# Kernel optimization log

Measured on AMD Instinct MI355X. Metric: run time of the kernel, lower is better.

The kernel has to match this reference:

```python
import jax, jax.numpy as jnp
import numpy as np

D_MODEL = 1024
NUM_HEADS = 16
ROPE_BASE = 10000.0


def _rope_sincos(T, head_dim, dtype):
    # angles[t, i] = t / base**(2i/head_dim), i in [0, head_dim//2)
    pos = jnp.arange(T, dtype=jnp.float32)[:, None]              # [T, 1]
    inv_freq = 1.0 / (ROPE_BASE ** (jnp.arange(0, head_dim, 2, dtype=jnp.float32) / head_dim))
    angles = pos * inv_freq                                       # [T, half]
    sin = jnp.sin(angles).astype(dtype)[None, :, None, :]         # [1, T, 1, half]
    cos = jnp.cos(angles).astype(dtype)[None, :, None, :]
    return sin, cos


def _apply_rope(x, sin, cos):
    # x: [B, T, H, head_dim]; deinterleave even/odd lanes, rotate, concat halves
    x1, x2 = x[..., ::2], x[..., 1::2]                            # [B, T, H, half] each
    return jnp.concatenate([x1 * cos - x2 * sin, x1 * sin + x2 * cos], axis=-1)


def setup_inputs() -> dict:
    key = jax.random.key(0)
    ks = jax.random.split(key, 5)
    B, T, D = 2, 2048, D_MODEL
    s = 0.02
    return {
        "x": jax.random.normal(ks[0], (B, T, D), dtype=jnp.float32),
        "w_qkv": jax.random.normal(ks[1], (3 * D, D), dtype=jnp.float32) * s,
        "b_qkv": jnp.zeros((3 * D,), dtype=jnp.float32),
        "w_out": jax.random.normal(ks[2], (D, D), dtype=jnp.float32) * s,
        "b_out": jnp.zeros((D,), dtype=jnp.float32),
    }


def reference(x, w_qkv, b_qkv, w_out, b_out):
    B, T, D = x.shape
    H = NUM_HEADS
    hd = D // H
    scale = hd ** -0.5

    qkv = (x @ w_qkv.T + b_qkv).reshape(B, T, 3, H, hd)
    q, k, v = qkv[:, :, 0], qkv[:, :, 1], qkv[:, :, 2]            # [B, T, H, hd]

    sin, cos = _rope_sincos(T, hd, x.dtype)
    q = _apply_rope(q, sin, cos)
    k = _apply_rope(k, sin, cos)

    scores = jnp.einsum("bthd,bshd->bhts", q, k) * scale          # [B, H, T, T]
    weights = jax.nn.softmax(scores, axis=-1)
    out = jnp.einsum("bhts,bshd->bthd", weights, v)               # [B, T, H, hd]
    out = out.reshape(B, T, D)
    return out @ w_out.T + b_out
```

## Files before the change

kernel.cpp:

```cpp
#include <hip/hip_runtime.h>
#include <cstdint>
#include <cstddef>

typedef __attribute__((ext_vector_type(8))) short short8;
typedef __attribute__((ext_vector_type(8))) __bf16 bf16x8;
typedef __attribute__((ext_vector_type(4))) float f32x4;
typedef __attribute__((ext_vector_type(16))) float f32x16;
typedef __attribute__((ext_vector_type(4))) unsigned int uint32x4;

#define LOG2E 1.44269504088896340736f

__device__ __forceinline__ unsigned short f2bf(float f) {
    unsigned int u = __builtin_bit_cast(unsigned int, f);
    u += 0x7fffu + ((u >> 16) & 1u);
    return (unsigned short)(u >> 16);
}

__device__ __forceinline__ f32x4 zero4() {
    f32x4 z; z.x = 0.f; z.y = 0.f; z.z = 0.f; z.w = 0.f; return z;
}
__device__ __forceinline__ f32x16 zero16() {
    f32x16 z;
    #pragma unroll
    for (int i = 0; i < 16; ++i) z[i] = 0.f;
    return z;
}

__device__ __forceinline__ f32x4 mfma16(short8 a, short8 b, f32x4 c) {
    return __builtin_amdgcn_mfma_f32_16x16x32_bf16(
        __builtin_bit_cast(bf16x8, a), __builtin_bit_cast(bf16x8, b), c, 0, 0, 0);
}
__device__ __forceinline__ f32x16 mfma32(short8 a, short8 b, f32x16 c) {
    return __builtin_amdgcn_mfma_f32_32x32x16_bf16(
        __builtin_bit_cast(bf16x8, a), __builtin_bit_cast(bf16x8, b), c, 0, 0, 0);
}

__device__ __forceinline__ unsigned int cvt_pk_bf16(float lo, float hi) {
    unsigned int r;
    asm("v_cvt_pk_bf16_f32 %0, %1, %2" : "=v"(r) : "v"(lo), "v"(hi));
    return r;
}

__device__ __forceinline__ uint2 permswap(unsigned x, unsigned y) {
#if __has_builtin(__builtin_amdgcn_permlane32_swap)
    auto r = __builtin_amdgcn_permlane32_swap(x, y, false, false);
    return make_uint2(r[0], r[1]);
#else
    int lane = threadIdx.x & 63;
    unsigned sy = __shfl_xor(y, 32), sx = __shfl_xor(x, 32);
    return make_uint2((lane < 32) ? x : sy, (lane < 32) ? sx : y);
#endif
}
__device__ __forceinline__ float red_max32(float v) {
    unsigned u = __builtin_bit_cast(unsigned, v);
    uint2 p = permswap(u, u);
    return fmaxf(__builtin_bit_cast(float, p.x), __builtin_bit_cast(float, p.y));
}

__device__ __forceinline__ void gload_lds16(const void* g, void* l, int lane) {
#if __has_builtin(__builtin_amdgcn_global_load_lds)
    __builtin_amdgcn_global_load_lds(
        (const __attribute__((address_space(1))) void*)g,
        (__attribute__((address_space(3))) void*)l, 16, 0, 0);
    (void)lane;
#else
    reinterpret_cast<int4*>(l)[lane] = *reinterpret_cast<const int4*>(g);
#endif
}

__global__ __launch_bounds__(256) void prep_kernel(
    const float* __restrict__ x, const float* __restrict__ wq,
    const float* __restrict__ wo,
    unsigned short* __restrict__ xb, unsigned short* __restrict__ wqb,
    unsigned short* __restrict__ wob, float2* __restrict__ tab) {
    const int S0 = 1048576, S1 = 786432, S2 = 262144;
    int i = blockIdx.x * 256 + threadIdx.x;
    const float* src; unsigned short* dst; int j;
    if (i < S0) { src = x; dst = xb; j = i; }
    else if (i < S0 + S1) { src = wq; dst = wqb; j = i - S0; }
    else if (i < S0 + S1 + S2) { src = wo; dst = wob; j = i - S0 - S1; }
    else {
        int idx = i - (S0 + S1 + S2);
        if (idx < 2048 * 32) {
            int t = idx >> 5, ii = idx & 31;
            float inv_freq = powf(10000.0f, -(float)ii / 32.0f);
            float ang = (float)t * inv_freq;
            tab[idx] = make_float2(cosf(ang), sinf(ang));
        }
        return;
    }
    float4 v = reinterpret_cast<const float4*>(src)[j];
    ushort4 o;
    o.x = f2bf(v.x); o.y = f2bf(v.y); o.z = f2bf(v.z); o.w = f2bf(v.w);
    reinterpret_cast<ushort4*>(dst)[j] = o;
}

template<int BM, int BN, int WMG, int WNG>
__device__ __forceinline__ void gemm_mainloop(
    const unsigned short* __restrict__ A, const unsigned short* __restrict__ B,
    int K, int m0, int n0, char* As, char* Bs,
    f32x4 (&acc)[BM / (WMG * 16)][BN / (WNG * 16)]) {
    constexpr int MT = BM / (WMG * 16), NTT = BN / (WNG * 16);
    constexpr int CA = BM / 64, CB = BN / 64;
    constexpr int ABUF = BM * 128, BBUF = BN * 128;
    int tid = threadIdx.x;
    int wave = tid >> 6, lane = tid & 63;
    int wm = wave / WNG, wn = wave % WNG;
    int g = lane >> 4, c = lane & 15;
    const int NS = K >> 6;

    auto stage = [&](int buf, int k0) {
        #pragma unroll
        for (int i = 0; i < CA; ++i) {
            int call = wave * CA + i;
            int s = call * 64 + lane;
            int row = s >> 3, c8 = s & 7;
            int csw = (c8 ^ (row & 7)) << 3;
            gload_lds16(A + (size_t)(m0 + row) * K + k0 + csw,
                        As + buf * ABUF + call * 1024, lane);
        }
        #pragma unroll
        for (int i = 0; i < CB; ++i) {
            int call = wave * CB + i;
            int s = call * 64 + lane;
            int row = s >> 3, c8 = s & 7;
            int csw = (c8 ^ (row & 7)) << 3;
            gload_lds16(B + (size_t)(n0 + row) * K + k0 + csw,
                        Bs + buf * BBUF + call * 1024, lane);
        }
    };

    stage(0, 0);

    #pragma unroll 1
    for (int t = 0; t < NS; ++t) {
        int cur = t & 1;
        asm volatile("s_waitcnt vmcnt(0)" ::: "memory");
        __builtin_amdgcn_s_barrier();
        __builtin_amdgcn_sched_barrier(0);
        if (t + 1 < NS) stage(cur ^ 1, (t + 1) * 64);

        const char* Ac = As + cur * ABUF;
        const char* Bc = Bs + cur * BBUF;
        #pragma unroll
        for (int kg = 0; kg < 2; ++kg) {
            short8 af[MT], bfr[NTT];
            #pragma unroll
            for (int mt = 0; mt < MT; ++mt) {
                int row = wm * (BM / WMG) + mt * 16 + c;
                af[mt] = *reinterpret_cast<const short8*>(Ac +
                    ((row * 128 + kg * 64 + g * 16) ^ ((row & 7) << 4)));
            }
            #pragma unroll
            for (int nt = 0; nt < NTT; ++nt) {
                int row = wn * (BN / WNG) + nt * 16 + c;
                bfr[nt] = *reinterpret_cast<const short8*>(Bc +
                    ((row * 128 + kg * 64 + g * 16) ^ ((row & 7) << 4)));
            }
            __builtin_amdgcn_s_setprio(1);
            #pragma unroll
            for (int mt = 0; mt < MT; ++mt)
                #pragma unroll
                for (int nt = 0; nt < NTT; ++nt)
                    acc[mt][nt] = mfma16(af[mt], bfr[nt], acc[mt][nt]);
            __builtin_amdgcn_s_setprio(0);
        }
    }
}

__global__ __launch_bounds__(512, 2) void qkv_gemm_kernel(
    const unsigned short* __restrict__ X, const unsigned short* __restrict__ W,
    const float* __restrict__ bias, const float2* __restrict__ tab,
    unsigned short* __restrict__ q, unsigned short* __restrict__ k,
    unsigned short* __restrict__ vt) {
    __shared__ char smem[80 * 1024];
    const int K = 1024;
    const float SCL = 0.125f * LOG2E;
    int flat = blockIdx.x;
    int swzb = (flat & 7) * 64 + (flat >> 3);
    int m0 = (swzb >> 4) * 128, n0 = (swzb & 15) * 192;
    f32x4 acc[2][6];
    #pragma unroll
    for (int i = 0; i < 2; ++i)
        #pragma unroll
        for (int j = 0; j < 6; ++j) acc[i][j] = zero4();

    gemm_mainloop<128, 192, 4, 2>(X, W, K, m0, n0, smem, smem + 32768, acc);

    int tid = threadIdx.x;
    int wave = tid >> 6, lane = tid & 63;
    int wm = wave >> 1, wn = wave & 1;
    int g = lane >> 4, c = lane & 15;
    int mbase = m0 + wm * 32, nbase = n0 + wn * 96;
    #pragma unroll
    for (int mt = 0; mt < 2; ++mt) {
        #pragma unroll
        for (int nt = 0; nt < 6; ++nt) {
            f32x4 a = acc[mt][nt];
            int n = nbase + nt * 16 + c;
            int s = n >> 10;
            int h = (n >> 6) & 15;
            int d = n & 63;
            float bn = bias[n];
            #pragma unroll
            for (int r = 0; r < 4; ++r) {
                int m = mbase + mt * 16 + g * 4 + r;
                int bb = m >> 11, t = m & 2047;
                float val = a[r] + bn;
                float partner = __shfl_xor(val, 1);
                int bh = bb * 16 + h;
                if (s == 2) {
                    vt[((size_t)bh * 64 + d) * 2048 + t] = f2bf(val);
                } else {
                    int i2 = d >> 1;
                    float2 cs = tab[t * 32 + i2];
                    float outv; int dout;
                    if ((d & 1) == 0) { outv = val * cs.x - partner * cs.y; dout = i2; }
                    else              { outv = partner * cs.y + val * cs.x; dout = 32 + i2; }
                    if (s == 0) outv *= SCL;
                    (s == 0 ? q : k)[((size_t)bh * 2048 + t) * 64 + dout] = f2bf(outv);
                }
            }
        }
    }
}

__global__ __launch_bounds__(256, 2) void attn_kernel(
    const unsigned short* __restrict__ Q, const unsigned short* __restrict__ Kin,
    const unsigned short* __restrict__ VT, unsigned short* __restrict__ O) {
    __shared__ int4 smem4[65536 / 16];
    char* smem = (char*)smem4;
    const int T = 2048, NT = 16;
    int flat = blockIdx.x + 16 * blockIdx.y;
    int swzb = (flat & 7) * 64 + (flat >> 3);
    int bh = swzb >> 4;
    int qt = swzb & 15;
    int tid = threadIdx.x, wave = tid >> 6, lane = tid & 63;
    int lam = lane & 31, hi = lane >> 5;
    int q = qt * 128 + wave * 32 + lam;

    const unsigned short* Qb = Q + ((size_t)bh * T + q) * 64;
    const unsigned short* Kb = Kin + (size_t)bh * T * 64;
    const unsigned short* VTb = VT + (size_t)bh * 64 * T;

    uint32x4 qtmp[4];
    #pragma unroll
    for (int c4 = 0; c4 < 4; ++c4)
        qtmp[c4] = *reinterpret_cast<const uint32x4*>(Qb + c4 * 16 + hi * 8);
    #pragma unroll
    for (int c4 = 0; c4 < 4; ++c4)
        asm volatile("" : "+v"(qtmp[c4]));
    short8 qf[4];
    #pragma unroll
    for (int c4 = 0; c4 < 4; ++c4) qf[c4] = __builtin_bit_cast(short8, qtmp[c4]);

    short8 ones;
    #pragma unroll
    for (int i = 0; i < 8; ++i) ones[i] = (short)0x3F80;

    f32x16 o0 = zero16(), o1 = zero16(), lacc = zero16();
    float m_run = -1e30f;
    int swz = (lam & 7) << 4;

    char* KsB = smem;
    char* VsB = smem + 32768;

    auto stage = [&](int buf, int t) {
        int j0 = t * 128;
        #pragma unroll
        for (int st = 0; st < 2; ++st) {
            #pragma unroll
            for (int i = 0; i < 2; ++i) {
                int call = wave * 2 + i;
                int s = call * 64 + lane;
                int row = s >> 3, c8 = s & 7;
                int csw = (c8 ^ (row & 7)) << 3;
                gload_lds16(Kb + (size_t)(j0 + st * 64 + row) * 64 + csw,
                            KsB + buf * 16384 + st * 8192 + call * 1024, lane);
                gload_lds16(VTb + (size_t)row * T + j0 + st * 64 + csw,
                            VsB + buf * 16384 + st * 8192 + call * 1024, lane);
            }
        }
    };

    auto subtile = [&](const char* Kc, const char* Vc) {
        f32x16 s0 = zero16(), s1 = zero16();
        __builtin_amdgcn_s_setprio(1);
        #pragma unroll
        for (int c4 = 0; c4 < 4; ++c4) {
            int col = c4 * 32 + hi * 16;
            short8 kf0 = *reinterpret_cast<const short8*>(Kc + ((lam * 128 + col) ^ swz));
            s0 = mfma32(kf0, qf[c4], s0);
            short8 kf1 = *reinterpret_cast<const short8*>(Kc + (((lam + 32) * 128 + col) ^ swz));
            s1 = mfma32(kf1, qf[c4], s1);
        }
        __builtin_amdgcn_s_setprio(0);

        float tm = fmaxf(s0[0], s1[0]);
        #pragma unroll
        for (int r = 1; r < 16; ++r) tm = fmaxf(tm, fmaxf(s0[r], s1[r]));
        float tmax = red_max32(tm);
        if (__any(tmax - m_run > 8.0f)) {
            float mnew = fmaxf(m_run, tmax);
            float alpha = exp2f(m_run - mnew);
            m_run = mnew;
            #pragma unroll
            for (int r = 0; r < 16; ++r) {
                o0[r] *= alpha; o1[r] *= alpha; lacc[r] *= alpha;
            }
        }
        float p0[16], p1[16];
        #pragma unroll
        for (int r = 0; r < 16; ++r) p0[r] = exp2f(s0[r] - m_run);
        #pragma unroll
        for (int r = 0; r < 16; ++r) p1[r] = exp2f(s1[r] - m_run);

        short8 pa[4];
        #pragma unroll
        for (int blk = 0; blk < 2; ++blk) {
            const float* p = blk ? p1 : p0;
            #pragma unroll
            for (int jt = 0; jt < 2; ++jt) {
                unsigned a0 = cvt_pk_bf16(p[jt * 8 + 0], p[jt * 8 + 1]);
                unsigned a1 = cvt_pk_bf16(p[jt * 8 + 2], p[jt * 8 + 3]);
                unsigned b0 = cvt_pk_bf16(p[jt * 8 + 4], p[jt * 8 + 5]);
                unsigned b1 = cvt_pk_bf16(p[jt * 8 + 6], p[jt * 8 + 7]);
                uint2 pr0 = permswap(a0, b0);
                uint2 pr1 = permswap(a1, b1);
                uint4 w;
                w.x = pr0.x;
                w.y = pr1.x;
                w.z = pr0.y;
                w.w = pr1.y;
                pa[blk * 2 + jt] = __builtin_bit_cast(short8, w);
            }
        }

        __builtin_amdgcn_s_setprio(1);
        #pragma unroll
        for (int jt = 0; jt < 4; ++jt) {
            int col = jt * 32 + hi * 16;
            short8 vf0 = *reinterpret_cast<const short8*>(Vc + ((lam * 128 + col) ^ swz));
            o0 = mfma32(vf0, pa[jt], o0);
            short8 vf1 = *reinterpret_cast<const short8*>(Vc + (((lam + 32) * 128 + col) ^ swz));
            o1 = mfma32(vf1, pa[jt], o1);
            lacc = mfma32(ones, pa[jt], lacc);
        }
        __builtin_amdgcn_s_setprio(0);
    };

    stage(0, 0);

    #pragma unroll 1
    for (int t = 0; t < NT; ++t) {
        int cur = t & 1;
        asm volatile("s_waitcnt vmcnt(0)" ::: "memory");
        __builtin_amdgcn_s_barrier();
        __builtin_amdgcn_sched_barrier(0);
        if (t + 1 < NT) stage(cur ^ 1, t + 1);

        subtile(KsB + cur * 16384, VsB + cur * 16384);
        subtile(KsB + cur * 16384 + 8192, VsB + cur * 16384 + 8192);
    }

    float l_run = lacc[0];

    float rinv = 1.0f / l_run;
    int b_ = bh >> 4, h_ = bh & 15;
    unsigned short* Orow = O + ((size_t)(b_ * 2048) + q) * 1024 + h_ * 64;
    #pragma unroll
    for (int rq = 0; rq < 4; ++rq) {
        ushort4 w0, w1;
        w0.x = f2bf(o0[rq * 4 + 0] * rinv);
        w0.y = f2bf(o0[rq * 4 + 1] * rinv);
        w0.z = f2bf(o0[rq * 4 + 2] * rinv);
        w0.w = f2bf(o0[rq * 4 + 3] * rinv);
        w1.x = f2bf(o1[rq * 4 + 0] * rinv);
        w1.y = f2bf(o1[rq * 4 + 1] * rinv);
        w1.z = f2bf(o1[rq * 4 + 2] * rinv);
        w1.w = f2bf(o1[rq * 4 + 3] * rinv);
        int d0 = rq * 8 + hi * 4;
        *reinterpret_cast<ushort4*>(Orow + d0) = w0;
        *reinterpret_cast<ushort4*>(Orow + 32 + d0) = w1;
    }
}

__global__ __launch_bounds__(512, 2) void out_gemm_kernel(
    const unsigned short* __restrict__ Aattn, const unsigned short* __restrict__ W,
    const float* __restrict__ bias, float* __restrict__ out) {
    __shared__ char smem[48 * 1024];
    const int K = 1024, N = 1024;
    int flat = blockIdx.x;
    int swzb = (flat & 7) * 64 + (flat >> 3);
    int m0 = (swzb & 63) * 64, n0 = (swzb >> 6) * 128;
    f32x4 acc[2][2];
    #pragma unroll
    for (int i = 0; i < 2; ++i)
        #pragma unroll
        for (int j = 0; j < 2; ++j) acc[i][j] = zero4();

    gemm_mainloop<64, 128, 2, 4>(Aattn, W, K, m0, n0, smem, smem + 16384, acc);

    int tid = threadIdx.x;
    int wave = tid >> 6, lane = tid & 63;
    int wm = wave >> 2, wn = wave & 3;
    int g = lane >> 4, c = lane & 15;
    int mbase = m0 + wm * 32, nbase = n0 + wn * 32;
    #pragma unroll
    for (int mt = 0; mt < 2; ++mt)
        #pragma unroll
        for (int nt = 0; nt < 2; ++nt) {
            int n = nbase + nt * 16 + c;
            float bn = bias[n];
            #pragma unroll
            for (int r = 0; r < 4; ++r) {
                int m = mbase + mt * 16 + g * 4 + r;
                out[(size_t)m * N + n] = acc[mt][nt][r] + bn;
            }
        }
}

extern "C" void kernel_launch(void* const* d_in, const int* in_sizes, int n_in,
                              void* d_out, int out_size, void* d_ws, size_t ws_size,
                              hipStream_t stream) {
    (void)in_sizes; (void)n_in; (void)out_size; (void)ws_size;
    const float* x     = (const float*)d_in[0];
    const float* w_qkv = (const float*)d_in[1];
    const float* b_qkv = (const float*)d_in[2];
    const float* w_out = (const float*)d_in[3];
    const float* b_out = (const float*)d_in[4];
    float* out = (float*)d_out;

    const int B = 2, T = 2048, D = 1024;
    const int M = B * T;
    const size_t MB = 1024 * 1024;
    (void)D; (void)M;

    char* ws = (char*)d_ws;
    unsigned short* xb    = (unsigned short*)(ws);
    unsigned short* wqkvb = (unsigned short*)(ws + 8 * MB);
    unsigned short* woutb = (unsigned short*)(ws + 14 * MB);
    unsigned short* qb    = (unsigned short*)(ws + 16 * MB);
    unsigned short* kb    = (unsigned short*)(ws + 24 * MB);
    unsigned short* vtb   = (unsigned short*)(ws + 32 * MB);
    unsigned short* attnb = (unsigned short*)(ws + 40 * MB);
    float2* tab           = (float2*)(ws + 48 * MB);

    prep_kernel<<<dim3((2097152 + 65536) / 256), dim3(256), 0, stream>>>(
        x, w_qkv, w_out, xb, wqkvb, woutb, tab);
    qkv_gemm_kernel<<<dim3(512), dim3(512), 0, stream>>>(xb, wqkvb, b_qkv, tab, qb, kb, vtb);
    attn_kernel<<<dim3(T / 128, B * 16), dim3(256), 0, stream>>>(qb, kb, vtb, attnb);
    out_gemm_kernel<<<dim3(512), dim3(512), 0, stream>>>(attnb, woutb, b_out, out);
}
```

Baseline: 140.1 us.

## Merge two 64-key subtiles into one 128-key softmax step with V prefetch

Replaces the two sequential 64-key subtile calls per staged tile with a single 128-key step. All four score MFMA groups are issued together and one row-max reduction and rescale check covers the whole tile. The first half of the V fragments is loaded from LDS before the softmax math so the load latency overlaps with the exp and convert work. This halves the cross-lane max reductions and branch checks per tile, but it raises register pressure (four score accumulators, p arrays, eight V fragments), which may reduce occupancy or cause spills.

```diff
diff --git a/kernel.cpp b/kernel.cpp
--- a/kernel.cpp
+++ b/kernel.cpp
@@ -283,72 +283,6 @@
         }
     };
 
-    auto subtile = [&](const char* Kc, const char* Vc) {
-        f32x16 s0 = zero16(), s1 = zero16();
-        __builtin_amdgcn_s_setprio(1);
-        #pragma unroll
-        for (int c4 = 0; c4 < 4; ++c4) {
-            int col = c4 * 32 + hi * 16;
-            short8 kf0 = *reinterpret_cast<const short8*>(Kc + ((lam * 128 + col) ^ swz));
-            s0 = mfma32(kf0, qf[c4], s0);
-            short8 kf1 = *reinterpret_cast<const short8*>(Kc + (((lam + 32) * 128 + col) ^ swz));
-            s1 = mfma32(kf1, qf[c4], s1);
-        }
-        __builtin_amdgcn_s_setprio(0);
-
-        float tm = fmaxf(s0[0], s1[0]);
-        #pragma unroll
-        for (int r = 1; r < 16; ++r) tm = fmaxf(tm, fmaxf(s0[r], s1[r]));
-        float tmax = red_max32(tm);
-        if (__any(tmax - m_run > 8.0f)) {
-            float mnew = fmaxf(m_run, tmax);
-            float alpha = exp2f(m_run - mnew);
-            m_run = mnew;
-            #pragma unroll
-            for (int r = 0; r < 16; ++r) {
-                o0[r] *= alpha; o1[r] *= alpha; lacc[r] *= alpha;
-            }
-        }
-        float p0[16], p1[16];
-        #pragma unroll
-        for (int r = 0; r < 16; ++r) p0[r] = exp2f(s0[r] - m_run);
-        #pragma unroll
-        for (int r = 0; r < 16; ++r) p1[r] = exp2f(s1[r] - m_run);
-
-        short8 pa[4];
-        #pragma unroll
-        for (int blk = 0; blk < 2; ++blk) {
-            const float* p = blk ? p1 : p0;
-            #pragma unroll
-            for (int jt = 0; jt < 2; ++jt) {
-                unsigned a0 = cvt_pk_bf16(p[jt * 8 + 0], p[jt * 8 + 1]);
-                unsigned a1 = cvt_pk_bf16(p[jt * 8 + 2], p[jt * 8 + 3]);
-                unsigned b0 = cvt_pk_bf16(p[jt * 8 + 4], p[jt * 8 + 5]);
-                unsigned b1 = cvt_pk_bf16(p[jt * 8 + 6], p[jt * 8 + 7]);
-                uint2 pr0 = permswap(a0, b0);
-                uint2 pr1 = permswap(a1, b1);
-                uint4 w;
-                w.x = pr0.x;
-                w.y = pr1.x;
-                w.z = pr0.y;
-                w.w = pr1.y;
-                pa[blk * 2 + jt] = __builtin_bit_cast(short8, w);
-            }
-        }
-
-        __builtin_amdgcn_s_setprio(1);
-        #pragma unroll
-        for (int jt = 0; jt < 4; ++jt) {
-            int col = jt * 32 + hi * 16;
-            short8 vf0 = *reinterpret_cast<const short8*>(Vc + ((lam * 128 + col) ^ swz));
-            o0 = mfma32(vf0, pa[jt], o0);
-            short8 vf1 = *reinterpret_cast<const short8*>(Vc + (((lam + 32) * 128 + col) ^ swz));
-            o1 = mfma32(vf1, pa[jt], o1);
-            lacc = mfma32(ones, pa[jt], lacc);
-        }
-        __builtin_amdgcn_s_setprio(0);
-    };
-
     stage(0, 0);
 
     #pragma unroll 1
@@ -359,8 +293,102 @@
         __builtin_amdgcn_sched_barrier(0);
         if (t + 1 < NT) stage(cur ^ 1, t + 1);
 
-        subtile(KsB + cur * 16384, VsB + cur * 16384);
-        subtile(KsB + cur * 16384 + 8192, VsB + cur * 16384 + 8192);
+        const char* Kc = KsB + cur * 16384;
+        const char* Vc = VsB + cur * 16384;
+
+        f32x16 s0 = zero16(), s1 = zero16(), s2 = zero16(), s3 = zero16();
+        __builtin_amdgcn_s_setprio(1);
+        #pragma unroll
+        for (int c4 = 0; c4 < 4; ++c4) {
+            int col = c4 * 32 + hi * 16;
+            short8 kf;
+            kf = *reinterpret_cast<const short8*>(Kc + ((lam * 128 + col) ^ swz));
+            s0 = mfma32(kf, qf[c4], s0);
+            kf = *reinterpret_cast<const short8*>(Kc + (((lam + 32) * 128 + col) ^ swz));
+            s1 = mfma32(kf, qf[c4], s1);
+            kf = *reinterpret_cast<const short8*>(Kc + 8192 + ((lam * 128 + col) ^ swz));
+            s2 = mfma32(kf, qf[c4], s2);
+            kf = *reinterpret_cast<const short8*>(Kc + 8192 + (((lam + 32) * 128 + col) ^ swz));
+            s3 = mfma32(kf, qf[c4], s3);
+        }
+        __builtin_amdgcn_s_setprio(0);
+
+        short8 vf[8];
+        #pragma unroll
+        for (int jt = 0; jt < 4; ++jt) {
+            int col = jt * 32 + hi * 16;
+            vf[jt * 2]     = *reinterpret_cast<const short8*>(Vc + ((lam * 128 + col) ^ swz));
+            vf[jt * 2 + 1] = *reinterpret_cast<const short8*>(Vc + (((lam + 32) * 128 + col) ^ swz));
+        }
+
+        float mx[16];
+        #pragma unroll
+        for (int r = 0; r < 16; ++r)
+            mx[r] = fmaxf(fmaxf(s0[r], s1[r]), fmaxf(s2[r], s3[r]));
+        float tm = mx[0];
+        #pragma unroll
+        for (int r = 1; r < 16; ++r) tm = fmaxf(tm, mx[r]);
+        float tmax = red_max32(tm);
+        if (__any(tmax - m_run > 8.0f)) {
+            float mnew = fmaxf(m_run, tmax);
+            float alpha = exp2f(m_run - mnew);
+            m_run = mnew;
+            #pragma unroll
+            for (int r = 0; r < 16; ++r) {
+                o0[r] *= alpha; o1[r] *= alpha; lacc[r] *= alpha;
+            }
+        }
+        float p0[16], p1[16], p2[16], p3[16];
+        #pragma unroll
+        for (int r = 0; r < 16; ++r) p0[r] = exp2f(s0[r] - m_run);
+        #pragma unroll
+        for (int r = 0; r < 16; ++r) p1[r] = exp2f(s1[r] - m_run);
+        #pragma unroll
+        for (int r = 0; r < 16; ++r) p2[r] = exp2f(s2[r] - m_run);
+        #pragma unroll
+        for (int r = 0; r < 16; ++r) p3[r] = exp2f(s3[r] - m_run);
+
+        short8 pa[8];
+        {
+            const float* ps[4] = { p0, p1, p2, p3 };
+            #pragma unroll
+            for (int blk = 0; blk < 4; ++blk) {
+                const float* p = ps[blk];
+                #pragma unroll
+                for (int jt = 0; jt < 2; ++jt) {
+                    unsigned a0 = cvt_pk_bf16(p[jt * 8 + 0], p[jt * 8 + 1]);
+                    unsigned a1 = cvt_pk_bf16(p[jt * 8 + 2], p[jt * 8 + 3]);
+                    unsigned b0 = cvt_pk_bf16(p[jt * 8 + 4], p[jt * 8 + 5]);
+                    unsigned b1 = cvt_pk_bf16(p[jt * 8 + 6], p[jt * 8 + 7]);
+                    uint2 pr0 = permswap(a0, b0);
+                    uint2 pr1 = permswap(a1, b1);
+                    uint4 w;
+                    w.x = pr0.x;
+                    w.y = pr1.x;
+                    w.z = pr0.y;
+                    w.w = pr1.y;
+                    pa[blk * 2 + jt] = __builtin_bit_cast(short8, w);
+                }
+            }
+        }
+
+        __builtin_amdgcn_s_setprio(1);
+        #pragma unroll
+        for (int jt = 0; jt < 4; ++jt) {
+            o0 = mfma32(vf[jt * 2], pa[jt], o0);
+            o1 = mfma32(vf[jt * 2 + 1], pa[jt], o1);
+            lacc = mfma32(ones, pa[jt], lacc);
+        }
+        #pragma unroll
+        for (int jt = 0; jt < 4; ++jt) {
+            int col = jt * 32 + hi * 16;
+            short8 vg0 = *reinterpret_cast<const short8*>(Vc + 8192 + ((lam * 128 + col) ^ swz));
+            o0 = mfma32(vg0, pa[4 + jt], o0);
+            short8 vg1 = *reinterpret_cast<const short8*>(Vc + 8192 + (((lam + 32) * 128 + col) ^ swz));
+            o1 = mfma32(vg1, pa[4 + jt], o1);
+            lacc = mfma32(ones, pa[4 + jt], lacc);
+        }
+        __builtin_amdgcn_s_setprio(0);
     }
 
     float l_run = lacc[0];
```

After: 138.8 us. No clear change (-1.0%).
